# Kernel optimization log

Hardware: AMD Instinct MI355X
Metric: run time of the kernel (lower is better)

The kernel has to match this reference:

```python
import jax, jax.numpy as jnp
import numpy as np
from jax import lax

N, T, H, E = 50000, 200, 128, 1600000


def setup_inputs() -> dict:
    key = jax.random.key(0)
    ks = jax.random.split(key, 32)
    s = 0.05
    inp = {}
    inp["lightcurve"] = jax.random.normal(ks[0], (N, T), dtype=jnp.float32)
    inp["edge_index"] = jax.random.randint(ks[1], (2, E), 0, N, dtype=jnp.int32)
    # LSTM layer 0 (input_dim=1) and layer 1 (input H), PyTorch gate order i,f,g,o
    inp["W_ih0"] = jax.random.normal(ks[2], (4 * H, 1), jnp.float32) * s
    inp["W_hh0"] = jax.random.normal(ks[3], (4 * H, H), jnp.float32) * s
    inp["b_ih0"] = jnp.zeros((4 * H,), jnp.float32)
    inp["b_hh0"] = jnp.zeros((4 * H,), jnp.float32)
    inp["W_ih1"] = jax.random.normal(ks[4], (4 * H, H), jnp.float32) * s
    inp["W_hh1"] = jax.random.normal(ks[5], (4 * H, H), jnp.float32) * s
    inp["b_ih1"] = jnp.zeros((4 * H,), jnp.float32)
    inp["b_hh1"] = jnp.zeros((4 * H,), jnp.float32)
    # 3 GCN conv layers + LayerNorms
    for i in range(3):
        inp[f"Wg{i}"] = jax.random.normal(ks[6 + i], (H, H), jnp.float32) * s
        inp[f"bg{i}"] = jnp.zeros((H,), jnp.float32)
        inp[f"gamma{i}"] = jnp.ones((H,), jnp.float32)
        inp[f"beta{i}"] = jnp.zeros((H,), jnp.float32)
    inp["W_out"] = jax.random.normal(ks[10], (H, 1), jnp.float32) * s
    inp["b_out"] = jnp.zeros((1,), jnp.float32)
    return inp


def _lstm_encode(x, W_ih0, W_hh0, b_ih0, b_hh0, W_ih1, W_hh1, b_ih1, b_hh1):
    # x: [N, T, 1] -> final hidden of layer 2: [N, H]. Both layers fused in one scan.
    n = x.shape[0]
    h = W_hh0.shape[1]

    def cell(xt, hs, cs, Wih, Whh, bih, bhh):
        g = xt @ Wih.T + hs @ Whh.T + (bih + bhh)
        i, f, gg, o = jnp.split(g, 4, axis=-1)
        cs = jax.nn.sigmoid(f) * cs + jax.nn.sigmoid(i) * jnp.tanh(gg)
        hs = jax.nn.sigmoid(o) * jnp.tanh(cs)
        return hs, cs

    def step(carry, x_t):
        h1, c1, h2, c2 = carry
        h1, c1 = cell(x_t, h1, c1, W_ih0, W_hh0, b_ih0, b_hh0)
        h2, c2 = cell(h1, h2, c2, W_ih1, W_hh1, b_ih1, b_hh1)
        return (h1, c1, h2, c2), None

    z = jnp.zeros((n, h), x.dtype)
    (_, _, h2, _), _ = lax.scan(step, (z, z, z, z), jnp.swapaxes(x, 0, 1))
    return h2


def _forward(lightcurve, W_ih0, W_hh0, b_ih0, b_hh0, W_ih1, W_hh1, b_ih1, b_hh1,
             Wg0, bg0, gamma0, beta0, Wg1, bg1, gamma1, beta1, Wg2, bg2, gamma2, beta2,
             W_out, b_out, edge_index):
    n = lightcurve.shape[0]
    h = _lstm_encode(lightcurve[..., None], W_ih0, W_hh0, b_ih0, b_hh0,
                     W_ih1, W_hh1, b_ih1, b_hh1)
    # GCN normalization (PyG GCNConv defaults: add self-loops, symmetric norm)
    loops = jnp.arange(n, dtype=edge_index.dtype)
    row = jnp.concatenate([edge_index[0], loops])  # source
    col = jnp.concatenate([edge_index[1], loops])  # target
    deg = jax.ops.segment_sum(jnp.ones_like(col, dtype=h.dtype), col, num_segments=n)
    dinv = lax.rsqrt(jnp.maximum(deg, 1.0))
    enorm = dinv[row] * dinv[col]  # [E+N]
    for Wg, bg, gm, bt in ((Wg0, bg0, gamma0, beta0), (Wg1, bg1, gamma1, beta1), (Wg2, bg2, gamma2, beta2)):
        h_prev = h
        msg = (h @ Wg)[row] * enorm[:, None]            # gather + scale
        h = jax.ops.segment_sum(msg, col, num_segments=n) + bg  # scatter-add
        mu = h.mean(-1, keepdims=True)                  # LayerNorm
        var = jnp.mean((h - mu) ** 2, axis=-1, keepdims=True)
        h = (h - mu) * lax.rsqrt(var + 1e-5) * gm + bt
        h = jax.nn.relu(h)
        h = h + h_prev  # dropout is identity in eval mode
    pooled = h.mean(axis=0, keepdims=True)  # [1, H]
    return pooled @ W_out + b_out           # [1, 1]


def reference(lightcurve, edge_index, W_ih0, W_hh0, b_ih0, b_hh0,
              W_ih1, W_hh1, b_ih1, b_hh1,
              Wg0, bg0, gamma0, beta0, Wg1, bg1, gamma1, beta1,
              Wg2, bg2, gamma2, beta2, W_out, b_out):
    return _forward(lightcurve, W_ih0, W_hh0, b_ih0, b_hh0, W_ih1, W_hh1, b_ih1, b_hh1,
                    Wg0, bg0, gamma0, beta0, Wg1, bg1, gamma1, beta1,
                    Wg2, bg2, gamma2, beta2, W_out, b_out, edge_index)
```

## Files before the change

### kernel.cpp

```cpp
#include <hip/hip_runtime.h>

#define NN 50000
#define TT 200
#define HH 128
#define EE 1600000

#define NL2E  -1.4426950408889634f
#define TWOL2E 2.8853900817779268f

#define STR 152

typedef _Float16 f16x8 __attribute__((ext_vector_type(8)));
typedef float f32x4 __attribute__((ext_vector_type(4)));

__device__ __forceinline__ float sg2(float x) {
    return __builtin_amdgcn_rcpf(1.f + exp2f(x));
}
__device__ __forceinline__ float th2(float x) {
    return 1.f - 2.f * __builtin_amdgcn_rcpf(exp2f(x) + 1.f);
}
__device__ __forceinline__ f32x4 sg2_4(f32x4 x) {
    f32x4 r; r[0] = sg2(x[0]); r[1] = sg2(x[1]); r[2] = sg2(x[2]); r[3] = sg2(x[3]); return r;
}
__device__ __forceinline__ f32x4 th2_4(f32x4 x) {
    f32x4 r; r[0] = th2(x[0]); r[1] = th2(x[1]); r[2] = th2(x[2]); r[3] = th2(x[3]); return r;
}
__device__ __forceinline__ f32x4 splat4(float s) { f32x4 r = {s, s, s, s}; return r; }
__device__ __forceinline__ unsigned short f2h_bits(float x) {
    _Float16 h = (_Float16)x;
    union { _Float16 h; unsigned short u; } cv; cv.h = h; return cv.u;
}
__device__ __forceinline__ float h2f_bits(unsigned short u) {
    union { _Float16 h; unsigned short u; } cv; cv.u = u; return (float)cv.h;
}

__global__ void pack_w(const float* __restrict__ W, unsigned short* __restrict__ out) {
    int tile = blockIdx.x;
    int jn = tile >> 2, kk = tile & 3;
    int L = threadIdx.x;
    int n = jn * 16 + (L & 15);
    int k0 = kk * 32 + (L >> 4) * 8;
    float sc = ((jn >> 3) == 2) ? TWOL2E : NL2E;
    unsigned short* dst = out + (size_t)tile * 512 + L * 8;
#pragma unroll
    for (int i = 0; i < 8; ++i) dst[i] = f2h_bits(W[n * 128 + k0 + i] * sc);
}

__global__ void bias_prep(const float* __restrict__ bih0, const float* __restrict__ bhh0,
                          const float* __restrict__ bih1, const float* __restrict__ bhh1,
                          const float* __restrict__ wih0,
                          float* __restrict__ b0g, float* __restrict__ b1g, float* __restrict__ wxg) {
    int i = blockIdx.x * 256 + threadIdx.x;
    if (i < 512) {
        float sc = ((i >> 7) == 2) ? TWOL2E : NL2E;
        b0g[i] = (bih0[i] + bhh0[i]) * sc;
        b1g[i] = (bih1[i] + bhh1[i]) * sc;
        wxg[i] = wih0[i] * sc;
    }
}

__global__ void transpose_lc(const float* __restrict__ lc, float* __restrict__ xT) {
    __shared__ float tile[32][33];
    int tx = threadIdx.x, ty = threadIdx.y;
    int n0 = blockIdx.y * 32, t0 = blockIdx.x * 32;
#pragma unroll
    for (int i = 0; i < 32; i += 8) {
        int n = n0 + ty + i, t = t0 + tx;
        if (n < NN && t < TT) tile[ty + i][tx] = lc[(size_t)n * TT + t];
    }
    __syncthreads();
#pragma unroll
    for (int i = 0; i < 32; i += 8) {
        int t = t0 + ty + i, n = n0 + tx;
        if (n < NN && t < TT) xT[(size_t)t * NN + n] = tile[tx][ty + i];
    }
}


#define MFMA16(A, B, C) __builtin_amdgcn_mfma_f32_16x16x32_f16((A), (B), (C), 0, 0, 0)

#define LDW(V, BASE, G, KK) \
    const f16x8 V = *reinterpret_cast<const f16x8*>((BASE) + (size_t)((G) * 8 + w) * 2048 + (KK) * 512 + lane * 8);

#define MMCR(HB, BI, BF, BG, BO, KK) {                                         \
    f16x8 a0_ = *reinterpret_cast<const f16x8*>(&(HB)[col][(KK) * 32 + quad * 8]);      \
    f16x8 a1_ = *reinterpret_cast<const f16x8*>(&(HB)[16 + col][(KK) * 32 + quad * 8]); \
    aI0 = MFMA16(a0_, BI, aI0); aI1 = MFMA16(a1_, BI, aI1);                    \
    aF0 = MFMA16(a0_, BF, aF0); aF1 = MFMA16(a1_, BF, aF1);                    \
    aG0 = MFMA16(a0_, BG, aG0); aG1 = MFMA16(a1_, BG, aG1);                    \
    aO0 = MFMA16(a0_, BO, aO0); aO1 = MFMA16(a1_, BO, aO1);                    \
}

#define ACT0N(RT, C, H, AI, AF, AG, AO) {                                      \
    f32x4 xv_ = *reinterpret_cast<const f32x4*>(&xs[(RT) * 16 + quad * 4]);    \
    f32x4 gi_ = AI + splat4(bI) + xv_ * splat4(wI);                            \
    f32x4 gf_ = AF + splat4(bF) + xv_ * splat4(wF);                            \
    f32x4 gg_ = AG + splat4(bG) + xv_ * splat4(wG);                            \
    f32x4 go_ = AO + splat4(bO) + xv_ * splat4(wO);                            \
    C = sg2_4(gf_) * C + sg2_4(gi_) * th2_4(gg_);                              \
    H = sg2_4(go_) * th2_4(C * splat4(TWOL2E));                                \
}

#define ACT1N(C, H, AI, AF, AG, AO) {                                          \
    f32x4 gi_ = AI + splat4(bI);                                               \
    f32x4 gf_ = AF + splat4(bF);                                               \
    f32x4 gg_ = AG + splat4(bG);                                               \
    f32x4 go_ = AO + splat4(bO);                                               \
    C = sg2_4(gf_) * C + sg2_4(gi_) * th2_4(gg_);                              \
    H = sg2_4(go_) * th2_4(C * splat4(TWOL2E));                                \
}

#define WRH(HB, RT, H)                                                         \
    (HB)[(RT) * 16 + quad * 4 + 0][j_] = f2h_bits((H)[0]);                     \
    (HB)[(RT) * 16 + quad * 4 + 1][j_] = f2h_bits((H)[1]);                     \
    (HB)[(RT) * 16 + quad * 4 + 2][j_] = f2h_bits((H)[2]);                     \
    (HB)[(RT) * 16 + quad * 4 + 3][j_] = f2h_bits((H)[3]);

#define STEP(PB, RB, T)                                                        \
    {                      \
        f32x4 aI0 = {}, aI1 = {}, aF0 = {}, aF1 = {};                          \
        f32x4 aG0 = {}, aG1 = {}, aO0 = {}, aO1 = {};                          \
        MMCR(h1s[RB], pI0, pF0, pG0, pO0, 0)                                   \
        MMCR(h1s[RB], pI1, pF1, pG1, pO1, 1)                                   \
        MMCR(h1s[RB], pI2, pF2, pG2, pO2, 2)                                   \
        MMCR(h1s[RB], pI3, pF3, pG3, pO3, 3)                                   \
        const float bI = b0s[j_], bF = b0s[128 + j_];                          \
        const float bG = b0s[256 + j_], bO = b0s[384 + j_];                    \
        const float wI = wxs[j_], wF = wxs[128 + j_];                          \
        const float wG = wxs[256 + j_], wO = wxs[384 + j_];                    \
        f32x4 h1v0, h1v1;                                                      \
        ACT0N(0, c1_0, h1v0, aI0, aF0, aG0, aO0)                               \
        ACT0N(1, c1_1, h1v1, aI1, aF1, aG1, aO1)                               \
        WRH(h1s[PB], 0, h1v0)                                                  \
        WRH(h1s[PB], 1, h1v1)                                                  \
    }                                                                          \
    __syncthreads();                                                           \
    {             \
        f32x4 aI0 = {}, aI1 = {}, aF0 = {}, aF1 = {};                          \
        f32x4 aG0 = {}, aG1 = {}, aO0 = {}, aO1 = {};                          \
        MMCR(h1s[PB], uI0, uF0, uG0, uO0, 0)                                   \
        MMCR(h1s[PB], uI1, uF1, uG1, uO1, 1)                                   \
        MMCR(h1s[PB], uI2, uF2, uG2, uO2, 2)                                   \
        MMCR(h1s[PB], uI3, uF3, uG3, uO3, 3)                                   \
        MMCR(h2s[RB], vI0, vF0, vG0, vO0, 0)                                   \
        MMCR(h2s[RB], vI1, vF1, vG1, vO1, 1)                                   \
        MMCR(h2s[RB], vI2, vF2, vG2, vO2, 2)                                   \
        MMCR(h2s[RB], vI3, vF3, vG3, vO3, 3)                                   \
        if (tid < 32) {                    \
            int n_ = n0 + tid;                                                 \
            xs[tid] = ((T) + 1 < TT && n_ < NN)                                \
                          ? xT[(size_t)((T) + 1) * NN + n_] : 0.f;             \
        }                                                                      \
        const float bI = b1s[j_], bF = b1s[128 + j_];                          \
        const float bG = b1s[256 + j_], bO = b1s[384 + j_];                    \
        f32x4 h2v0, h2v1;                                                      \
        ACT1N(c2_0, h2v0, aI0, aF0, aG0, aO0)                                  \
        ACT1N(c2_1, h2v1, aI1, aF1, aG1, aO1)                                  \
        WRH(h2s[PB], 0, h2v0)                                                  \
        WRH(h2s[PB], 1, h2v1)                                                  \
    }                                                                          \
    __syncthreads();

__global__ __launch_bounds__(512, 2) void lstm_kernel(
    const float* __restrict__ xT,
    const unsigned short* __restrict__ w0p,
    const unsigned short* __restrict__ w1ip,
    const unsigned short* __restrict__ w1hp,
    const float* __restrict__ b0g, const float* __restrict__ b1g,
    const float* __restrict__ wxg,
    float* __restrict__ h2out) {
    __shared__ unsigned short h1s[2][32][STR];
    __shared__ unsigned short h2s[2][32][STR];
    __shared__ __align__(16) float xs[32];
    __shared__ float b0s[512], b1s[512], wxs[512];

    const int tid = threadIdx.x;
    const int w = tid >> 6;
    const int lane = tid & 63;
    const int col = lane & 15;
    const int quad = lane >> 4;
    const int n0 = blockIdx.x * 32;
    const int j_ = w * 16 + col;

    for (int i = tid; i < 2 * 32 * STR; i += 512) {
        (&h1s[0][0][0])[i] = 0; (&h2s[0][0][0])[i] = 0;
    }
    b0s[tid] = b0g[tid]; b1s[tid] = b1g[tid]; wxs[tid] = wxg[tid];
    if (tid < 32) { int n = n0 + tid; xs[tid] = (n < NN) ? xT[n] : 0.f; }

    LDW(pI0, w0p, 0, 0) LDW(pI1, w0p, 0, 1) LDW(pI2, w0p, 0, 2) LDW(pI3, w0p, 0, 3)
    LDW(pF0, w0p, 1, 0) LDW(pF1, w0p, 1, 1) LDW(pF2, w0p, 1, 2) LDW(pF3, w0p, 1, 3)
    LDW(pG0, w0p, 2, 0) LDW(pG1, w0p, 2, 1) LDW(pG2, w0p, 2, 2) LDW(pG3, w0p, 2, 3)
    LDW(pO0, w0p, 3, 0) LDW(pO1, w0p, 3, 1) LDW(pO2, w0p, 3, 2) LDW(pO3, w0p, 3, 3)
    LDW(uI0, w1ip, 0, 0) LDW(uI1, w1ip, 0, 1) LDW(uI2, w1ip, 0, 2) LDW(uI3, w1ip, 0, 3)
    LDW(uF0, w1ip, 1, 0) LDW(uF1, w1ip, 1, 1) LDW(uF2, w1ip, 1, 2) LDW(uF3, w1ip, 1, 3)
    LDW(uG0, w1ip, 2, 0) LDW(uG1, w1ip, 2, 1) LDW(uG2, w1ip, 2, 2) LDW(uG3, w1ip, 2, 3)
    LDW(uO0, w1ip, 3, 0) LDW(uO1, w1ip, 3, 1) LDW(uO2, w1ip, 3, 2) LDW(uO3, w1ip, 3, 3)
    LDW(vI0, w1hp, 0, 0) LDW(vI1, w1hp, 0, 1) LDW(vI2, w1hp, 0, 2) LDW(vI3, w1hp, 0, 3)
    LDW(vF0, w1hp, 1, 0) LDW(vF1, w1hp, 1, 1) LDW(vF2, w1hp, 1, 2) LDW(vF3, w1hp, 1, 3)
    LDW(vG0, w1hp, 2, 0) LDW(vG1, w1hp, 2, 1) LDW(vG2, w1hp, 2, 2) LDW(vG3, w1hp, 2, 3)
    LDW(vO0, w1hp, 3, 0) LDW(vO1, w1hp, 3, 1) LDW(vO2, w1hp, 3, 2) LDW(vO3, w1hp, 3, 3)

    f32x4 c1_0 = {}, c1_1 = {}, c2_0 = {}, c2_1 = {};

    __syncthreads();

#pragma unroll 1
    for (int tt = 0; tt < TT; tt += 2) {
        STEP(0, 1, tt)
        STEP(1, 0, tt + 1)
    }

    for (int i = tid; i < 32 * 128; i += 512) {
        int m = i >> 7, j = i & 127;
        int n = n0 + m;
        if (n < NN) h2out[(size_t)n * HH + j] = h2f_bits(h2s[1][m][j]);
    }
}

__global__ void deg_init(float* __restrict__ deg) {
    int i = blockIdx.x * 256 + threadIdx.x;
    if (i < NN) deg[i] = 1.f;
}
__global__ void deg_edges(const int* __restrict__ ei, float* __restrict__ deg) {
    int e = blockIdx.x * 256 + threadIdx.x;
    if (e < EE) unsafeAtomicAdd(&deg[ei[EE + e]], 1.f);
}
__global__ void dinv_k(const float* __restrict__ deg, float* __restrict__ dinv) {
    int i = blockIdx.x * 256 + threadIdx.x;
    if (i < NN) dinv[i] = rsqrtf(fmaxf(deg[i], 1.f));
}

__global__ void scan_off(const float* __restrict__ deg, int* __restrict__ off) {
    __shared__ int sp[256];
    const int tid = threadIdx.x;
    const int chunk = (NN + 255) / 256;
    const int i0 = tid * chunk;
    int s = 0;
    for (int i = 0; i < chunk; ++i) {
        int idx = i0 + i;
        if (idx < NN) s += (int)deg[idx] - 1;
    }
    sp[tid] = s;
    __syncthreads();
    for (int o = 1; o < 256; o <<= 1) {
        int v = (tid >= o) ? sp[tid - o] : 0;
        __syncthreads();
        sp[tid] += v;
        __syncthreads();
    }
    int run = sp[tid] - s;
    for (int i = 0; i < chunk; ++i) {
        int idx = i0 + i;
        if (idx < NN) { off[idx] = run; run += (int)deg[idx] - 1; }
    }
    if (tid == 255) off[NN] = sp[255];
}

__global__ void csr_fill(const int* __restrict__ ei, const float* __restrict__ dinv,
                         const int* __restrict__ off, int* __restrict__ cur,
                         int* __restrict__ crow, float* __restrict__ cw) {
    int e = blockIdx.x * 256 + threadIdx.x;
    if (e >= EE) return;
    int r = ei[e], c = ei[EE + e];
    int p = atomicAdd(&cur[c], 1);
    int idx = off[c] + p;
    crow[idx] = r;
    cw[idx] = dinv[r] * dinv[c];
}

__global__ void gcn_gemm(const float* __restrict__ h, const float* __restrict__ Wg,
                         float* __restrict__ hw) {
    __shared__ float hsT[128][36];
    int tid = threadIdx.x;
    int n0 = blockIdx.x * 32;
#pragma unroll
    for (int c = 0; c < 16; ++c) {
        int lin = c * 256 + tid;
        int m = lin >> 7, k = lin & 127;
        int n = n0 + m;
        hsT[k][m] = (n < NN) ? h[(size_t)n * HH + k] : 0.f;
    }
    __syncthreads();
    int j = tid & 127, p = tid >> 7;
    float acc[16];
#pragma unroll
    for (int m = 0; m < 16; ++m) acc[m] = 0.f;
    for (int k = 0; k < 128; ++k) {
        float wg = Wg[k * 128 + j];
        const float4* hp = reinterpret_cast<const float4*>(&hsT[k][p * 16]);
        float4 a = hp[0], b = hp[1], c = hp[2], d = hp[3];
        acc[0]  += a.x * wg; acc[1]  += a.y * wg; acc[2]  += a.z * wg; acc[3]  += a.w * wg;
        acc[4]  += b.x * wg; acc[5]  += b.y * wg; acc[6]  += b.z * wg; acc[7]  += b.w * wg;
        acc[8]  += c.x * wg; acc[9]  += c.y * wg; acc[10] += c.z * wg; acc[11] += c.w * wg;
        acc[12] += d.x * wg; acc[13] += d.y * wg; acc[14] += d.z * wg; acc[15] += d.w * wg;
    }
#pragma unroll
    for (int m = 0; m < 16; ++m) {
        int n = n0 + p * 16 + m;
        if (n < NN) hw[(size_t)n * HH + j] = acc[m];
    }
}

__global__ __launch_bounds__(256) void gcn_agg(
    const float* __restrict__ hw, const int* __restrict__ off,
    const int* __restrict__ crow, const float* __restrict__ cw,
    const float* __restrict__ dinv, const float* __restrict__ bg,
    const float* __restrict__ gamma, const float* __restrict__ beta,
    float* __restrict__ h) {
    __shared__ float xch[4][2];
    const int tid = threadIdx.x;
    const int half = tid >> 7;
    const int f = tid & 127;
    const int v = blockIdx.x * 2 + half;
    const float d = dinv[v];
    float acc = bg[f] + d * d * hw[v * HH + f];
    const int s1 = off[v + 1];
    for (int s = off[v]; s < s1; ++s) {
        int r = crow[s];
        float wv = cw[s];
        acc = fmaf(wv, hw[r * HH + f], acc);
    }
    float sum = acc, sq = acc * acc;
#pragma unroll
    for (int o = 32; o; o >>= 1) { sum += __shfl_xor(sum, o); sq += __shfl_xor(sq, o); }
    int wid = tid >> 6;
    if ((tid & 63) == 0) { xch[wid][0] = sum; xch[wid][1] = sq; }
    __syncthreads();
    sum += xch[wid ^ 1][0]; sq += xch[wid ^ 1][1];
    float mu = sum * (1.f / 128.f);
    float var = sq * (1.f / 128.f) - mu * mu;
    float rn = rsqrtf(var + 1e-5f);
    float o = (acc - mu) * rn * gamma[f] + beta[f];
    h[v * HH + f] = fmaxf(o, 0.f) + h[v * HH + f];
}

__global__ void pool_k(const float* __restrict__ h, float* __restrict__ pooled) {
    int j = threadIdx.x & 127, p = threadIdx.x >> 7;
    float s = 0.f;
    for (int n = blockIdx.x * 2 + p; n < NN; n += 512) s += h[(size_t)n * HH + j];
    unsafeAtomicAdd(&pooled[j], s);
}

__global__ void final_k(const float* __restrict__ pooled, const float* __restrict__ Wout,
                        const float* __restrict__ bout, float* __restrict__ out) {
    int lane = threadIdx.x;
    float s = pooled[lane] * Wout[lane] + pooled[lane + 64] * Wout[lane + 64];
#pragma unroll
    for (int o = 32; o; o >>= 1) s += __shfl_xor(s, o);
    if (lane == 0) out[0] = s * (1.f / (float)NN) + bout[0];
}

extern "C" void kernel_launch(void* const* d_in, const int* in_sizes, int n_in,
                              void* d_out, int out_size, void* d_ws, size_t ws_size,
                              hipStream_t stream) {
    const float* lc   = (const float*)d_in[0];
    const int*   ei   = (const int*)d_in[1];
    const float* Wih0 = (const float*)d_in[2];
    const float* Whh0 = (const float*)d_in[3];
    const float* bih0 = (const float*)d_in[4];
    const float* bhh0 = (const float*)d_in[5];
    const float* Wih1 = (const float*)d_in[6];
    const float* Whh1 = (const float*)d_in[7];
    const float* bih1 = (const float*)d_in[8];
    const float* bhh1 = (const float*)d_in[9];
    const float* Wout = (const float*)d_in[22];
    const float* bout = (const float*)d_in[23];
    float* out = (float*)d_out;

    float* ws   = (float*)d_ws;
    float* h    = ws;
    float* hw   = ws + 6400000;
    float* xT   = ws + 6400000;
    int*   off  = (int*)(ws + 12800000);
    int*   cur  = off + 50048;
    int*   crow = cur + 50048;
    float* cw   = (float*)(crow + EE);
    float* P      = ws + 16400064;
    float* deg    = P;
    float* dinv   = deg + 50000;
    float* b0g    = dinv + 50000;
    float* b1g    = b0g + 512;
    float* wxg    = b1g + 512;
    float* pooled = wxg + 512;
    unsigned short* w0p  = (unsigned short*)(pooled + 128);
    unsigned short* w1ip = w0p + 65536;
    unsigned short* w1hp = w1ip + 65536;

    pack_w<<<128, 64, 0, stream>>>(Whh0, w0p);
    pack_w<<<128, 64, 0, stream>>>(Wih1, w1ip);
    pack_w<<<128, 64, 0, stream>>>(Whh1, w1hp);
    bias_prep<<<2, 256, 0, stream>>>(bih0, bhh0, bih1, bhh1, Wih0, b0g, b1g, wxg);
    {
        dim3 g((TT + 31) / 32, (NN + 31) / 32), b(32, 8);
        transpose_lc<<<g, b, 0, stream>>>(lc, xT);
    }
    deg_init<<<(NN + 255) / 256, 256, 0, stream>>>(deg);
    deg_edges<<<(EE + 255) / 256, 256, 0, stream>>>(ei, deg);
    dinv_k<<<(NN + 255) / 256, 256, 0, stream>>>(deg, dinv);

    lstm_kernel<<<(NN + 31) / 32, 512, 0, stream>>>(xT, w0p, w1ip, w1hp, b0g, b1g, wxg, h);

    hipMemsetAsync(cur, 0, 50000 * sizeof(int), stream);
    scan_off<<<1, 256, 0, stream>>>(deg, off);
    csr_fill<<<(EE + 255) / 256, 256, 0, stream>>>(ei, dinv, off, cur, crow, cw);

    for (int l = 0; l < 3; ++l) {
        const float* Wg = (const float*)d_in[10 + 4 * l];
        const float* bg = (const float*)d_in[11 + 4 * l];
        const float* gm = (const float*)d_in[12 + 4 * l];
        const float* bt = (const float*)d_in[13 + 4 * l];
        gcn_gemm<<<(NN + 31) / 32, 256, 0, stream>>>(h, Wg, hw);
        gcn_agg<<<NN / 2, 256, 0, stream>>>(hw, off, crow, cw, dinv, bg, gm, bt, h);
    }

    hipMemsetAsync(pooled, 0, HH * sizeof(float), stream);
    pool_k<<<256, 256, 0, stream>>>(h, pooled);
    final_k<<<1, 64, 0, stream>>>(pooled, Wout, bout, out);
}
```

Baseline: 9.447 ms.

## Process 64 nodes per LSTM block, streaming weights from global instead of registers

Result: slower. 14.53 ms (+53.8%).

```diff
diff --git a/kernel.cpp b/kernel.cpp
--- a/kernel.cpp
+++ b/kernel.cpp
@@ -8,7 +8,7 @@
 #define NL2E  -1.4426950408889634f
 #define TWOL2E 2.8853900817779268f
 
-#define STR 152
+#define STR 136
 
 typedef _Float16 f16x8 __attribute__((ext_vector_type(8)));
 typedef float f32x4 __attribute__((ext_vector_type(4)));
@@ -79,33 +79,42 @@
 
 #define MFMA16(A, B, C) __builtin_amdgcn_mfma_f32_16x16x32_f16((A), (B), (C), 0, 0, 0)
 
-#define LDW(V, BASE, G, KK) \
-    const f16x8 V = *reinterpret_cast<const f16x8*>((BASE) + (size_t)((G) * 8 + w) * 2048 + (KK) * 512 + lane * 8);
-
-#define MMCR(HB, BI, BF, BG, BO, KK) {                                         \
+#define DECLACC(S) f32x4 aI0##S = {}, aI1##S = {}, aF0##S = {}, aF1##S = {}, \
+                         aG0##S = {}, aG1##S = {}, aO0##S = {}, aO1##S = {};
+
+#define MMCT(S, HB, KK, BI, BF, BG, BO) {                                      \
     f16x8 a0_ = *reinterpret_cast<const f16x8*>(&(HB)[col][(KK) * 32 + quad * 8]);      \
     f16x8 a1_ = *reinterpret_cast<const f16x8*>(&(HB)[16 + col][(KK) * 32 + quad * 8]); \
-    aI0 = MFMA16(a0_, BI, aI0); aI1 = MFMA16(a1_, BI, aI1);                    \
-    aF0 = MFMA16(a0_, BF, aF0); aF1 = MFMA16(a1_, BF, aF1);                    \
-    aG0 = MFMA16(a0_, BG, aG0); aG1 = MFMA16(a1_, BG, aG1);                    \
-    aO0 = MFMA16(a0_, BO, aO0); aO1 = MFMA16(a1_, BO, aO1);                    \
-}
-
-#define ACT0N(RT, C, H, AI, AF, AG, AO) {                                      \
-    f32x4 xv_ = *reinterpret_cast<const f32x4*>(&xs[(RT) * 16 + quad * 4]);    \
-    f32x4 gi_ = AI + splat4(bI) + xv_ * splat4(wI);                            \
-    f32x4 gf_ = AF + splat4(bF) + xv_ * splat4(wF);                            \
-    f32x4 gg_ = AG + splat4(bG) + xv_ * splat4(wG);                            \
-    f32x4 go_ = AO + splat4(bO) + xv_ * splat4(wO);                            \
+    aI0##S = MFMA16(a0_, BI, aI0##S); aI1##S = MFMA16(a1_, BI, aI1##S);        \
+    aF0##S = MFMA16(a0_, BF, aF0##S); aF1##S = MFMA16(a1_, BF, aF1##S);        \
+    aG0##S = MFMA16(a0_, BG, aG0##S); aG1##S = MFMA16(a1_, BG, aG1##S);        \
+    aO0##S = MFMA16(a0_, BO, aO0##S); aO1##S = MFMA16(a1_, BO, aO1##S);        \
+}
+
+#define MMC2(HA, HBT, PI, PF, PG, PO, KK) {                                    \
+    f16x8 bI_ = *reinterpret_cast<const f16x8*>((PI) + (KK) * 512);            \
+    f16x8 bF_ = *reinterpret_cast<const f16x8*>((PF) + (KK) * 512);            \
+    f16x8 bG_ = *reinterpret_cast<const f16x8*>((PG) + (KK) * 512);            \
+    f16x8 bO_ = *reinterpret_cast<const f16x8*>((PO) + (KK) * 512);            \
+    MMCT(A, HA, KK, bI_, bF_, bG_, bO_)                                        \
+    MMCT(B, HBT, KK, bI_, bF_, bG_, bO_)                                       \
+}
+
+#define ACT0N(RT, C, H, AI, AF, AG, AO, XO) {                                  \
+    f32x4 xv_ = *reinterpret_cast<const f32x4*>(&xs[(XO) + (RT) * 16 + quad * 4]); \
+    f32x4 gi_ = AI + splat4(B0I) + xv_ * splat4(WXI);                          \
+    f32x4 gf_ = AF + splat4(B0F) + xv_ * splat4(WXF);                          \
+    f32x4 gg_ = AG + splat4(B0G) + xv_ * splat4(WXG);                          \
+    f32x4 go_ = AO + splat4(B0O) + xv_ * splat4(WXO);                          \
     C = sg2_4(gf_) * C + sg2_4(gi_) * th2_4(gg_);                              \
     H = sg2_4(go_) * th2_4(C * splat4(TWOL2E));                                \
 }
 
 #define ACT1N(C, H, AI, AF, AG, AO) {                                          \
-    f32x4 gi_ = AI + splat4(bI);                                               \
-    f32x4 gf_ = AF + splat4(bF);                                               \
-    f32x4 gg_ = AG + splat4(bG);                                               \
-    f32x4 go_ = AO + splat4(bO);                                               \
+    f32x4 gi_ = AI + splat4(B1I);                                              \
+    f32x4 gf_ = AF + splat4(B1F);                                              \
+    f32x4 gg_ = AG + splat4(B1G);                                              \
+    f32x4 go_ = AO + splat4(B1O);                                              \
     C = sg2_4(gf_) * C + sg2_4(gi_) * th2_4(gg_);                              \
     H = sg2_4(go_) * th2_4(C * splat4(TWOL2E));                                \
 }
@@ -118,46 +127,46 @@
 
 #define STEP(PB, RB, T)                                                        \
     {                      \
-        f32x4 aI0 = {}, aI1 = {}, aF0 = {}, aF1 = {};                          \
-        f32x4 aG0 = {}, aG1 = {}, aO0 = {}, aO1 = {};                          \
-        MMCR(h1s[RB], pI0, pF0, pG0, pO0, 0)                                   \
-        MMCR(h1s[RB], pI1, pF1, pG1, pO1, 1)                                   \
-        MMCR(h1s[RB], pI2, pF2, pG2, pO2, 2)                                   \
-        MMCR(h1s[RB], pI3, pF3, pG3, pO3, 3)                                   \
-        const float bI = b0s[j_], bF = b0s[128 + j_];                          \
-        const float bG = b0s[256 + j_], bO = b0s[384 + j_];                    \
-        const float wI = wxs[j_], wF = wxs[128 + j_];                          \
-        const float wG = wxs[256 + j_], wO = wxs[384 + j_];                    \
-        f32x4 h1v0, h1v1;                                                      \
-        ACT0N(0, c1_0, h1v0, aI0, aF0, aG0, aO0)                               \
-        ACT0N(1, c1_1, h1v1, aI1, aF1, aG1, aO1)                               \
-        WRH(h1s[PB], 0, h1v0)                                                  \
-        WRH(h1s[PB], 1, h1v1)                                                  \
+        DECLACC(A) DECLACC(B)                                                  \
+        MMC2(h1sA[RB], h1sB[RB], p0I, p0F, p0G, p0O, 0)                        \
+        MMC2(h1sA[RB], h1sB[RB], p0I, p0F, p0G, p0O, 1)                        \
+        MMC2(h1sA[RB], h1sB[RB], p0I, p0F, p0G, p0O, 2)                        \
+        MMC2(h1sA[RB], h1sB[RB], p0I, p0F, p0G, p0O, 3)                        \
+        f32x4 h1v0A, h1v1A, h1v0B, h1v1B;                                      \
+        ACT0N(0, c1_0A, h1v0A, aI0A, aF0A, aG0A, aO0A, 0)                      \
+        ACT0N(1, c1_1A, h1v1A, aI1A, aF1A, aG1A, aO1A, 0)                      \
+        ACT0N(0, c1_0B, h1v0B, aI0B, aF0B, aG0B, aO0B, 32)                     \
+        ACT0N(1, c1_1B, h1v1B, aI1B, aF1B, aG1B, aO1B, 32)                     \
+        WRH(h1sA[PB], 0, h1v0A)                                                \
+        WRH(h1sA[PB], 1, h1v1A)                                                \
+        WRH(h1sB[PB], 0, h1v0B)                                                \
+        WRH(h1sB[PB], 1, h1v1B)                                                \
     }                                                                          \
     __syncthreads();                                                           \
     {             \
-        f32x4 aI0 = {}, aI1 = {}, aF0 = {}, aF1 = {};                          \
-        f32x4 aG0 = {}, aG1 = {}, aO0 = {}, aO1 = {};                          \
-        MMCR(h1s[PB], uI0, uF0, uG0, uO0, 0)                                   \
-        MMCR(h1s[PB], uI1, uF1, uG1, uO1, 1)                                   \
-        MMCR(h1s[PB], uI2, uF2, uG2, uO2, 2)                                   \
-        MMCR(h1s[PB], uI3, uF3, uG3, uO3, 3)                                   \
-        MMCR(h2s[RB], vI0, vF0, vG0, vO0, 0)                                   \
-        MMCR(h2s[RB], vI1, vF1, vG1, vO1, 1)                                   \
-        MMCR(h2s[RB], vI2, vF2, vG2, vO2, 2)                                   \
-        MMCR(h2s[RB], vI3, vF3, vG3, vO3, 3)                                   \
-        if (tid < 32) {                    \
+        DECLACC(A) DECLACC(B)                                                  \
+        MMC2(h1sA[PB], h1sB[PB], u0I, u0F, u0G, u0O, 0)                        \
+        MMC2(h1sA[PB], h1sB[PB], u0I, u0F, u0G, u0O, 1)                        \
+        MMC2(h1sA[PB], h1sB[PB], u0I, u0F, u0G, u0O, 2)                        \
+        MMC2(h1sA[PB], h1sB[PB], u0I, u0F, u0G, u0O, 3)                        \
+        MMC2(h2sA[RB], h2sB[RB], v0I, v0F, v0G, v0O, 0)                        \
+        MMC2(h2sA[RB], h2sB[RB], v0I, v0F, v0G, v0O, 1)                        \
+        MMC2(h2sA[RB], h2sB[RB], v0I, v0F, v0G, v0O, 2)                        \
+        MMC2(h2sA[RB], h2sB[RB], v0I, v0F, v0G, v0O, 3)                        \
+        if (tid < 64) {     \
             int n_ = n0 + tid;                                                 \
             xs[tid] = ((T) + 1 < TT && n_ < NN)                                \
                           ? xT[(size_t)((T) + 1) * NN + n_] : 0.f;             \
         }                                                                      \
-        const float bI = b1s[j_], bF = b1s[128 + j_];                          \
-        const float bG = b1s[256 + j_], bO = b1s[384 + j_];                    \
-        f32x4 h2v0, h2v1;                                                      \
-        ACT1N(c2_0, h2v0, aI0, aF0, aG0, aO0)                                  \
-        ACT1N(c2_1, h2v1, aI1, aF1, aG1, aO1)                                  \
-        WRH(h2s[PB], 0, h2v0)                                                  \
-        WRH(h2s[PB], 1, h2v1)                                                  \
+        f32x4 h2v0A, h2v1A, h2v0B, h2v1B;                                      \
+        ACT1N(c2_0A, h2v0A, aI0A, aF0A, aG0A, aO0A)                            \
+        ACT1N(c2_1A, h2v1A, aI1A, aF1A, aG1A, aO1A)                            \
+        ACT1N(c2_0B, h2v0B, aI0B, aF0B, aG0B, aO0B)                            \
+        ACT1N(c2_1B, h2v1B, aI1B, aF1B, aG1B, aO1B)                            \
+        WRH(h2sA[PB], 0, h2v0A)                                                \
+        WRH(h2sA[PB], 1, h2v1A)                                                \
+        WRH(h2sB[PB], 0, h2v0B)                                                \
+        WRH(h2sB[PB], 1, h2v1B)                                                \
     }                                                                          \
     __syncthreads();
 
@@ -169,39 +178,45 @@
     const float* __restrict__ b0g, const float* __restrict__ b1g,
     const float* __restrict__ wxg,
     float* __restrict__ h2out) {
-    __shared__ unsigned short h1s[2][32][STR];
-    __shared__ unsigned short h2s[2][32][STR];
-    __shared__ __align__(16) float xs[32];
-    __shared__ float b0s[512], b1s[512], wxs[512];
+    __shared__ unsigned short h1sA[2][32][STR];
+    __shared__ unsigned short h2sA[2][32][STR];
+    __shared__ unsigned short h1sB[2][32][STR];
+    __shared__ unsigned short h2sB[2][32][STR];
+    __shared__ __align__(16) float xs[64];
 
     const int tid = threadIdx.x;
     const int w = tid >> 6;
     const int lane = tid & 63;
     const int col = lane & 15;
     const int quad = lane >> 4;
-    const int n0 = blockIdx.x * 32;
+    const int n0 = blockIdx.x * 64;
     const int j_ = w * 16 + col;
 
     for (int i = tid; i < 2 * 32 * STR; i += 512) {
-        (&h1s[0][0][0])[i] = 0; (&h2s[0][0][0])[i] = 0;
-    }
-    b0s[tid] = b0g[tid]; b1s[tid] = b1g[tid]; wxs[tid] = wxg[tid];
-    if (tid < 32) { int n = n0 + tid; xs[tid] = (n < NN) ? xT[n] : 0.f; }
-
-    LDW(pI0, w0p, 0, 0) LDW(pI1, w0p, 0, 1) LDW(pI2, w0p, 0, 2) LDW(pI3, w0p, 0, 3)
-    LDW(pF0, w0p, 1, 0) LDW(pF1, w0p, 1, 1) LDW(pF2, w0p, 1, 2) LDW(pF3, w0p, 1, 3)
-    LDW(pG0, w0p, 2, 0) LDW(pG1, w0p, 2, 1) LDW(pG2, w0p, 2, 2) LDW(pG3, w0p, 2, 3)
-    LDW(pO0, w0p, 3, 0) LDW(pO1, w0p, 3, 1) LDW(pO2, w0p, 3, 2) LDW(pO3, w0p, 3, 3)
-    LDW(uI0, w1ip, 0, 0) LDW(uI1, w1ip, 0, 1) LDW(uI2, w1ip, 0, 2) LDW(uI3, w1ip, 0, 3)
-    LDW(uF0, w1ip, 1, 0) LDW(uF1, w1ip, 1, 1) LDW(uF2, w1ip, 1, 2) LDW(uF3, w1ip, 1, 3)
-    LDW(uG0, w1ip, 2, 0) LDW(uG1, w1ip, 2, 1) LDW(uG2, w1ip, 2, 2) LDW(uG3, w1ip, 2, 3)
-    LDW(uO0, w1ip, 3, 0) LDW(uO1, w1ip, 3, 1) LDW(uO2, w1ip, 3, 2) LDW(uO3, w1ip, 3, 3)
-    LDW(vI0, w1hp, 0, 0) LDW(vI1, w1hp, 0, 1) LDW(vI2, w1hp, 0, 2) LDW(vI3, w1hp, 0, 3)
-    LDW(vF0, w1hp, 1, 0) LDW(vF1, w1hp, 1, 1) LDW(vF2, w1hp, 1, 2) LDW(vF3, w1hp, 1, 3)
-    LDW(vG0, w1hp, 2, 0) LDW(vG1, w1hp, 2, 1) LDW(vG2, w1hp, 2, 2) LDW(vG3, w1hp, 2, 3)
-    LDW(vO0, w1hp, 3, 0) LDW(vO1, w1hp, 3, 1) LDW(vO2, w1hp, 3, 2) LDW(vO3, w1hp, 3, 3)
-
-    f32x4 c1_0 = {}, c1_1 = {}, c2_0 = {}, c2_1 = {};
+        (&h1sA[0][0][0])[i] = 0; (&h2sA[0][0][0])[i] = 0;
+        (&h1sB[0][0][0])[i] = 0; (&h2sB[0][0][0])[i] = 0;
+    }
+    if (tid < 64) { int n = n0 + tid; xs[tid] = (n < NN) ? xT[n] : 0.f; }
+
+    const float B0I = b0g[j_], B0F = b0g[128 + j_], B0G = b0g[256 + j_], B0O = b0g[384 + j_];
+    const float B1I = b1g[j_], B1F = b1g[128 + j_], B1G = b1g[256 + j_], B1O = b1g[384 + j_];
+    const float WXI = wxg[j_], WXF = wxg[128 + j_], WXG = wxg[256 + j_], WXO = wxg[384 + j_];
+
+    const unsigned short* p0I = w0p + (size_t)w * 2048 + lane * 8;
+    const unsigned short* p0F = w0p + (size_t)(8 + w) * 2048 + lane * 8;
+    const unsigned short* p0G = w0p + (size_t)(16 + w) * 2048 + lane * 8;
+    const unsigned short* p0O = w0p + (size_t)(24 + w) * 2048 + lane * 8;
+    const unsigned short* u0I = w1ip + (size_t)w * 2048 + lane * 8;
+    const unsigned short* u0F = w1ip + (size_t)(8 + w) * 2048 + lane * 8;
+    const unsigned short* u0G = w1ip + (size_t)(16 + w) * 2048 + lane * 8;
+    const unsigned short* u0O = w1ip + (size_t)(24 + w) * 2048 + lane * 8;
+    const unsigned short* v0I = w1hp + (size_t)w * 2048 + lane * 8;
+    const unsigned short* v0F = w1hp + (size_t)(8 + w) * 2048 + lane * 8;
+    const unsigned short* v0G = w1hp + (size_t)(16 + w) * 2048 + lane * 8;
+    const unsigned short* v0O = w1hp + (size_t)(24 + w) * 2048 + lane * 8;
+
+    f32x4 c1_0A = {}, c1_1A = {}, c2_0A = {}, c2_1A = {};
+    f32x4 c1_0B = {}, c1_1B = {}, c2_0B = {}, c2_1B = {};
 
     __syncthreads();
 
@@ -211,10 +226,13 @@
         STEP(1, 0, tt + 1)
     }
 
-    for (int i = tid; i < 32 * 128; i += 512) {
+    for (int i = tid; i < 64 * 128; i += 512) {
         int m = i >> 7, j = i & 127;
         int n = n0 + m;
-        if (n < NN) h2out[(size_t)n * HH + j] = h2f_bits(h2s[1][m][j]);
+        if (n < NN) {
+            unsigned short v = (m < 32) ? h2sA[1][m][j] : h2sB[1][m - 32][j];
+            h2out[(size_t)n * HH + j] = h2f_bits(v);
+        }
     }
 }
 
@@ -399,7 +417,7 @@
     deg_edges<<<(EE + 255) / 256, 256, 0, stream>>>(ei, deg);
     dinv_k<<<(NN + 255) / 256, 256, 0, stream>>>(deg, dinv);
 
-    lstm_kernel<<<(NN + 31) / 32, 512, 0, stream>>>(xT, w0p, w1ip, w1hp, b0g, b1g, wxg, h);
+    lstm_kernel<<<(NN + 63) / 64, 512, 0, stream>>>(xT, w0p, w1ip, w1hp, b0g, b1g, wxg, h);
 
     hipMemsetAsync(cur, 0, 50000 * sizeof(int), stream);
     scan_off<<<1, 256, 0, stream>>>(deg, off);
```
